# Kernel tuning notes

Hardware: AMD Instinct MI355X
Metric: run time of the kernel (lower is better)

Reference implementation:

```python
import jax, jax.numpy as jnp
import numpy as np

B = 8
INPUT_SIZE = 32        # fc output dim == res row length
RESAMPLING = 500       # chunk width; 500->250->125->62->31 under 4 stride-2 pools
CHUNKS = 15            # == channel_size; seq length T = CHUNKS * RESAMPLING
T = CHUNKS * RESAMPLING
EPS = 1e-5
FC_IN = 32 * 6 * 31    # 5952 = flattened (C,H,W) embedding output


def _conv2d(x, w, b, pad):
    y = jax.lax.conv_general_dilated(x, w, (1, 1), pad,
                                     dimension_numbers=('NCHW', 'OIHW', 'NCHW'))
    return y + b[None, :, None, None]


def _bn(x, g, beta, m, v):
    # eval-mode BatchNorm2d with running stats
    scale = g / jnp.sqrt(v + EPS)
    return (x - m[None, :, None, None]) * scale[None, :, None, None] + beta[None, :, None, None]


def _maxpool22(x):
    return jax.lax.reduce_window(x, -jnp.inf, jax.lax.max, (1, 1, 2, 2), (1, 1, 2, 2), 'VALID')


def _forward(x, w1, b1, g1, beta1, m1, v1, w2, b2, g2, beta2, m2, v2,
             w3, b3, g3, beta3, m3, v3, w4, b4, g4, beta4, m4, v4,
             wfc, bfc, wc3, bc3, wout, bout):
    bsz = x.shape[0]
    # Vectorize the original per-sample / per-chunk Python loops:
    # split each [100, T] sample into CHUNKS windows of width RESAMPLING.
    h = x[:, 0].reshape(bsz, 100, CHUNKS, RESAMPLING)
    h = h.transpose(0, 2, 1, 3).reshape(bsz * CHUNKS, 1, 100, RESAMPLING)
    for w, b, g, bt, m, v in ((w1, b1, g1, beta1, m1, v1),
                              (w2, b2, g2, beta2, m2, v2),
                              (w3, b3, g3, beta3, m3, v3),
                              (w4, b4, g4, beta4, m4, v4)):
        h = _maxpool22(jax.nn.relu(_bn(_conv2d(h, w, b, [(2, 2), (2, 2)]), g, bt, m, v)))
    feats = h.reshape(bsz * CHUNKS, FC_IN)          # torch flattens in (C,H,W) order
    res = feats @ wfc.T + bfc                       # [B*15, 32]
    r = res.reshape(bsz, CHUNKS, INPUT_SIZE)[..., None]  # [B, 15, 32, 1] (NCHW)

    pad_c = lambda t: jnp.pad(t, ((0, 0), (0, 0), (1, 1), (0, 0)))   # ZeroPad2d((0,0,1,1))
    conv3 = lambda t: _conv2d(t, wc3, bc3, [(0, 0), (0, 0)])          # (3,1) conv
    r = conv3(jax.nn.relu(pad_c(r)))
    r = conv3(jax.nn.relu(pad_c(r)))
    while r.shape[2] > 2:  # static shapes: H 32->16->8->4->2
        p = jnp.pad(r, ((0, 0), (0, 0), (0, 1), (0, 0)))              # ZeroPad2d((0,0,0,1))
        px = jax.lax.reduce_window(p, -jnp.inf, jax.lax.max, (1, 1, 3, 1), (1, 1, 2, 2), 'VALID')
        t = conv3(jax.nn.relu(pad_c(px)))
        t = conv3(jax.nn.relu(pad_c(t)))
        r = t + px
    return r.reshape(bsz, 2 * CHUNKS) @ wout.T + bout  # [B, 2]


def setup_inputs() -> dict:
    key = jax.random.key(0)
    ks = jax.random.split(key, 16)

    def rn(k, shape, s):
        return jax.random.normal(k, shape, jnp.float32) * s

    inp = {"x": jax.random.normal(ks[0], (B, 1, 100, T), jnp.float32)}
    chans = [(1, 16), (16, 32), (32, 64), (64, 32)]
    for i, (ci, co) in enumerate(chans, 1):
        inp[f"w{i}"] = rn(ks[i], (co, ci, 5, 5), (2.0 / (ci * 25)) ** 0.5)
        inp[f"b{i}"] = jnp.zeros((co,), jnp.float32)
        inp[f"g{i}"] = jnp.ones((co,), jnp.float32)
        inp[f"beta{i}"] = jnp.zeros((co,), jnp.float32)
        inp[f"m{i}"] = jnp.zeros((co,), jnp.float32)
        inp[f"v{i}"] = jnp.ones((co,), jnp.float32)
    inp["wfc"] = rn(ks[5], (INPUT_SIZE, FC_IN), FC_IN ** -0.5)
    inp["bfc"] = jnp.zeros((INPUT_SIZE,), jnp.float32)
    inp["wc3"] = rn(ks[6], (CHUNKS, CHUNKS, 3, 1), (CHUNKS * 3) ** -0.5)
    inp["bc3"] = jnp.zeros((CHUNKS,), jnp.float32)
    inp["wout"] = rn(ks[7], (2, 2 * CHUNKS), (2 * CHUNKS) ** -0.5)
    inp["bout"] = jnp.zeros((2,), jnp.float32)
    return inp


def reference(x, w1, b1, g1, beta1, m1, v1, w2, b2, g2, beta2, m2, v2,
              w3, b3, g3, beta3, m3, v3, w4, b4, g4, beta4, m4, v4,
              wfc, bfc, wc3, bc3, wout, bout):
    return _forward(x, w1, b1, g1, beta1, m1, v1, w2, b2, g2, beta2, m2, v2,
                    w3, b3, g3, beta3, m3, v3, w4, b4, g4, beta4, m4, v4,
                    wfc, bfc, wc3, bc3, wout, bout)
```

## Files before the change

### kernel.cpp

```cpp
#include <hip/hip_runtime.h>
#include <hip/hip_bf16.h>

#define EPS 1e-5f

typedef short bf16x8 __attribute__((ext_vector_type(8)));
typedef float f32x4  __attribute__((ext_vector_type(4)));

__device__ __forceinline__ unsigned short f2bf(float f) {
    __hip_bfloat16 h = __float2bfloat16(f);
    return *(unsigned short*)&h;
}
__device__ __forceinline__ float bf2f(unsigned short u) {
    __hip_bfloat16 h = *(__hip_bfloat16*)&u;
    return __bfloat162float(h);
}

__global__ void prep_scsh(
    const float* g1, const float* be1, const float* m1, const float* v1, const float* b1,
    const float* g2, const float* be2, const float* m2, const float* v2, const float* b2,
    const float* g3, const float* be3, const float* m3, const float* v3, const float* b3,
    const float* g4, const float* be4, const float* m4, const float* v4, const float* b4,
    float* base)
{
    const int t = threadIdx.x;
    if (t < 32) {
        const float sc = g2[t] / sqrtf(v2[t] + EPS);
        base[t] = sc; base[32 + t] = (b2[t] - m2[t]) * sc + be2[t];
    } else if (t < 96) {
        const int c = t - 32;
        const float sc = g3[c] / sqrtf(v3[c] + EPS);
        base[64 + c] = sc; base[128 + c] = (b3[c] - m3[c]) * sc + be3[c];
    } else if (t < 128) {
        const int c = t - 96;
        const float sc = g4[c] / sqrtf(v4[c] + EPS);
        base[192 + c] = sc; base[224 + c] = (b4[c] - m4[c]) * sc + be4[c];
    } else if (t < 144) {
        const int c = t - 128;
        const float sc = g1[c] / sqrtf(v1[c] + EPS);
        base[256 + c] = sc; base[272 + c] = (b1[c] - m1[c]) * sc + be1[c];
    }
}

template <int CI, int CO, int NP>
__global__ void prep_A(const float* __restrict__ w, unsigned short* __restrict__ Apk)
{
    constexpr int COTALL = CO / 16;
    const int tot = NP * COTALL * 512;
    for (int i = blockIdx.x * 256 + threadIdx.x; i < tot; i += gridDim.x * 256) {
        const int j = i & 7, lane = (i >> 3) & 63, pc = i >> 9;
        const int p = pc / COTALL, cot = pc % COTALL;
        const int kidx = p * 32 + (lane >> 4) * 8 + j;
        const int tap = kidx / CI, ci = kidx % CI;
        const int co = cot * 16 + (lane & 15);
        const float val = (tap < 25) ? w[((size_t)co * CI + ci) * 25 + tap] : 0.f;
        Apk[i] = f2bf(val);
    }
}

__global__ void prep_A1(const float* __restrict__ w, unsigned short* __restrict__ Apk)
{
    const int i = threadIdx.x;
    if (i < 512) {
        const int j = i & 7, lane = i >> 3;
        const int k = ((lane >> 4) & 3) * 8 + j;
        const int co = lane & 15;
        Apk[i] = f2bf((k < 25) ? w[co * 25 + k] : 0.f);
    }
}

__global__ void prep_fcw(const float* __restrict__ wfc, unsigned short* __restrict__ wfcT)
{
    for (int i = blockIdx.x * 256 + threadIdx.x; i < 32 * 5952; i += gridDim.x * 256) {
        const int o = i / 5952, j = i % 5952;
        const int c = j & 31, yx = j >> 5;
        wfcT[i] = f2bf(wfc[(size_t)o * 5952 + c * 186 + yx]);
    }
}

__global__ __launch_bounds__(256) void conv1_mfma(
    const float* __restrict__ x,
    const unsigned short* __restrict__ Apk1,
    const float* __restrict__ sc, const float* __restrict__ sh,
    unsigned short* __restrict__ out)
{
    constexpr int RSTR = 38;
    __shared__ unsigned short tile[12 * RSTR];
    const int n = blockIdx.z;
    const int y0 = blockIdx.y * 8, x0 = blockIdx.x * 32;
    const int b = n / 15, c = n % 15;
    const float* xb = x + (size_t)b * 100 * 7500 + (size_t)c * 500;
    const int tid = threadIdx.x;

    for (int i = tid; i < 12 * 36; i += 256) {
        const int yy = i / 36, xx = i % 36;
        const int gy = y0 - 2 + yy, gx = x0 - 2 + xx;
        float v = 0.f;
        if (gy >= 0 && gy < 100 && gx >= 0 && gx < 500) v = xb[gy * 7500 + gx];
        tile[yy * RSTR + xx] = f2bf(v);
    }

    const int lane = tid & 63, wav = tid >> 6;
    const int g = lane >> 4, c15 = lane & 15;
    const bf16x8 a = *(const bf16x8*)(Apk1 + lane * 8);

    int off[8]; unsigned short msk[8];
    #pragma unroll
    for (int j = 0; j < 8; ++j) {
        int tap = g * 8 + j;
        msk[j] = (tap < 25) ? 0xFFFFu : 0u;
        if (tap > 24) tap = 24;
        off[j] = (tap / 5) * RSTR + (tap % 5);
    }
    __syncthreads();

    f32x4 acc[2][2] = {};
    #pragma unroll
    for (int r = 0; r < 2; ++r)
        #pragma unroll
        for (int cg = 0; cg < 2; ++cg) {
            const int base = (2 * wav + r) * RSTR + cg * 16 + c15;
            bf16x8 bfrag;
            #pragma unroll
            for (int j = 0; j < 8; ++j) {
                const unsigned short v = tile[base + off[j]] & msk[j];
                ((unsigned short*)&bfrag)[j] = (short)v;
            }
            acc[r][cg] = __builtin_amdgcn_mfma_f32_16x16x32_bf16(a, bfrag, acc[r][cg], 0, 0, 0);
        }

    const int py = blockIdx.y * 4 + wav;
    const float4 scv = *(const float4*)(sc + g * 4);
    const float4 shv = *(const float4*)(sh + g * 4);
    #pragma unroll
    for (int cg = 0; cg < 2; ++cg) {
        const int px = (x0 >> 1) + cg * 8 + (c15 >> 1);
        ushort4 st;
        #pragma unroll
        for (int reg = 0; reg < 4; ++reg) {
            const float scr = (&scv.x)[reg], shr = (&shv.x)[reg];
            const float v0 = fmaxf(acc[0][cg][reg] * scr + shr, 0.f);
            const float v1 = fmaxf(acc[1][cg][reg] * scr + shr, 0.f);
            float mx = fmaxf(v0, v1);
            mx = fmaxf(mx, __shfl_xor(mx, 1));
            (&st.x)[reg] = f2bf(mx);
        }
        if ((lane & 1) == 0 && py < 50 && px < 250)
            *(ushort4*)(out + (((size_t)n * 50 + py) * 250 + px) * 16 + g * 4) = st;
    }
}

template <int CI, int CO, int H, int W, int PH, int PW, int NP>
__global__ __launch_bounds__(256) void mfma_conv(
    const unsigned short* __restrict__ in,
    const unsigned short* __restrict__ Apk,
    const float* __restrict__ sc, const float* __restrict__ sh,
    unsigned short* __restrict__ outp)
{
    constexpr int TH = 8, TW = 32, ROWS = TH + 4, COLS = TW + 4;
    constexpr int CSTR = CI * 2 + 16;
    constexpr int COTALL = CO / 16, COB = CO / 32;
    constexpr int CPC = CI / 8;
    __shared__ char smem[ROWS * COLS * CSTR];

    const int n = blockIdx.z / COB, cob = blockIdx.z % COB;
    const int ytile = blockIdx.y * TH, xtile = blockIdx.x * TW;
    const int tid = threadIdx.x;

    for (int i = tid; i < ROWS * COLS * CPC; i += 256) {
        const int cell = i / CPC, ch = i % CPC;
        const int yy = cell / COLS, xx = cell % COLS;
        const int gy = ytile - 2 + yy, gx = xtile - 2 + xx;
        uint4 val = make_uint4(0, 0, 0, 0);
        if (gy >= 0 && gy < H && gx >= 0 && gx < W)
            val = *(const uint4*)(in + ((((size_t)n * H + gy) * W + gx) * CI + ch * 8));
        *(uint4*)(smem + (size_t)(yy * COLS + xx) * CSTR + ch * 16) = val;
    }
    __syncthreads();

    const int lane = tid & 63, wav = tid >> 6;
    const int g = lane >> 4, c15 = lane & 15;
    const int laneCi = (CI == 16) ? ((g & 1) * 16) : (g * 16);
    const bool hi = (lane >= 32);

    int baddr[2][2];
    #pragma unroll
    for (int r = 0; r < 2; ++r)
        #pragma unroll
        for (int cg = 0; cg < 2; ++cg)
            baddr[r][cg] = ((wav * 2 + r) * COLS + cg * 16 + c15) * CSTR + laneCi;

    f32x4 acc[2][2][2] = {};

    #pragma unroll
    for (int p = 0; p < NP; ++p) {
        int D;
        if (CI == 16) {
            int t0 = p * 2;     if (t0 > 24) t0 = 24;
            int t1 = p * 2 + 1; if (t1 > 24) t1 = 24;
            const int D0 = ((t0 / 5) * COLS + t0 % 5) * CSTR;
            const int D1 = ((t1 / 5) * COLS + t1 % 5) * CSTR;
            D = hi ? D1 : D0;
        } else {
            const int tap = (CI == 32) ? p : (p >> 1);
            D = ((tap / 5) * COLS + tap % 5) * CSTR + ((CI == 64) ? (p & 1) * 64 : 0);
        }
        bf16x8 a[2], b[2][2];
        #pragma unroll
        for (int ct = 0; ct < 2; ++ct)
            a[ct] = *(const bf16x8*)(Apk + ((size_t)(p * COTALL + cob * 2 + ct) * 64 + lane) * 8);
        #pragma unroll
        for (int r = 0; r < 2; ++r)
            #pragma unroll
            for (int cg = 0; cg < 2; ++cg)
                b[r][cg] = *(const bf16x8*)(smem + baddr[r][cg] + D);
        #pragma unroll
        for (int r = 0; r < 2; ++r)
            #pragma unroll
            for (int ct = 0; ct < 2; ++ct)
                #pragma unroll
                for (int cg = 0; cg < 2; ++cg)
                    acc[r][ct][cg] = __builtin_amdgcn_mfma_f32_16x16x32_bf16(
                        a[ct], b[r][cg], acc[r][ct][cg], 0, 0, 0);
    }

    const int py = blockIdx.y * 4 + wav;
    #pragma unroll
    for (int ct = 0; ct < 2; ++ct) {
        const int coW = cob * 32 + ct * 16;
        const float4 scv = *(const float4*)(sc + coW + g * 4);
        const float4 shv = *(const float4*)(sh + coW + g * 4);
        #pragma unroll
        for (int cg = 0; cg < 2; ++cg) {
            const int px = (xtile >> 1) + cg * 8 + (c15 >> 1);
            ushort4 st;
            #pragma unroll
            for (int reg = 0; reg < 4; ++reg) {
                const float scr = (&scv.x)[reg], shr = (&shv.x)[reg];
                const float v0 = fmaxf(acc[0][ct][cg][reg] * scr + shr, 0.f);
                const float v1 = fmaxf(acc[1][ct][cg][reg] * scr + shr, 0.f);
                float mx = fmaxf(v0, v1);
                mx = fmaxf(mx, __shfl_xor(mx, 1));
                (&st.x)[reg] = f2bf(mx);
            }
            if ((lane & 1) == 0 && py < PH && px < PW)
                *(ushort4*)(outp + (((size_t)n * PH + py) * PW + px) * CO + coW + g * 4) = st;
        }
    }
}

__global__ __launch_bounds__(256) void fc_kernel(
    const unsigned short* __restrict__ feats, const unsigned short* __restrict__ wfcT,
    const float* __restrict__ bfc, float* __restrict__ res)
{
    const int n = blockIdx.x;
    const int lane = threadIdx.x & 63;
    const int wave = threadIdx.x >> 6;
    const unsigned short* f = feats + (size_t)n * 5952;
    #pragma unroll
    for (int o8 = 0; o8 < 8; ++o8) {
        const int o = wave * 8 + o8;
        const unsigned short* wr = wfcT + (size_t)o * 5952;
        float s = 0.f;
        #pragma unroll
        for (int i = 0; i < 12; ++i) {
            const int j8 = (i * 64 + lane) * 8;
            if (j8 < 5952) {
                const bf16x8 fv = *(const bf16x8*)(f + j8);
                const bf16x8 wv = *(const bf16x8*)(wr + j8);
                #pragma unroll
                for (int q = 0; q < 8; ++q)
                    s += bf2f(((const unsigned short*)&fv)[q]) *
                         bf2f(((const unsigned short*)&wv)[q]);
            }
        }
        #pragma unroll
        for (int off = 32; off > 0; off >>= 1) s += __shfl_down(s, off, 64);
        if (lane == 0) res[n * 32 + o] = s + bfc[o];
    }
}

__global__ __launch_bounds__(512) void dpcnn_kernel(
    const float* __restrict__ res,
    const float* __restrict__ wc3, const float* __restrict__ bc3,
    const float* __restrict__ wout, const float* __restrict__ bout,
    float* __restrict__ out)
{
    __shared__ float rr[8][15][32];
    __shared__ float ar[8][15][34];
    __shared__ float tr[8][15][34];
    __shared__ float px[8][15][16];
    __shared__ float wk[15][45];
    __shared__ float bk[15];

    const int tid = threadIdx.x;
    for (int i = tid; i < 15 * 45; i += 512) ((float*)wk)[i] = wc3[i];
    if (tid < 15) bk[tid] = bc3[tid];
    for (int i = tid; i < 8 * 15 * 32; i += 512) {
        const int h = i & 31, c = (i >> 5) % 15, b = i / 480;
        const float val = res[i];
        rr[b][c][h] = val;
        ar[b][c][h + 1] = fmaxf(val, 0.f);
    }
    for (int i = tid; i < 8 * 15; i += 512) {
        const int c = i % 15, b = i / 15;
        ar[b][c][0] = 0.f; ar[b][c][33] = 0.f;
        tr[b][c][0] = 0.f; tr[b][c][33] = 0.f;
    }
    __syncthreads();

    #define CONV45(SRC, BCH, CCH, HH)                                          \
        float s0 = bk[CCH], s1 = 0.f, s2 = 0.f;                                \
        {                                                                      \
            const float* srow = &SRC[BCH][0][HH];                              \
            const float* wrow = &wk[CCH][0];                                   \
            _Pragma("unroll")                                                  \
            for (int ci = 0; ci < 15; ++ci) {                                  \
                s0 += wrow[ci * 3 + 0] * srow[ci * 34 + 0];                    \
                s1 += wrow[ci * 3 + 1] * srow[ci * 34 + 1];                    \
                s2 += wrow[ci * 3 + 2] * srow[ci * 34 + 2];                    \
            }                                                                  \
        }                                                                      \
        const float val = s0 + s1 + s2;

    {
        for (int i = tid; i < 8 * 15 * 32; i += 512) {
            const int h = i & 31, cc = (i >> 5) % 15, b = i / 480;
            CONV45(ar, b, cc, h)
            tr[b][cc][h + 1] = fmaxf(val, 0.f);
        }
        __syncthreads();
        for (int i = tid; i < 8 * 15 * 32; i += 512) {
            const int h = i & 31, cc = (i >> 5) % 15, b = i / 480;
            CONV45(tr, b, cc, h)
            rr[b][cc][h] = val;
            ar[b][cc][h + 1] = fmaxf(val, 0.f);
        }
        __syncthreads();
    }

    for (int H = 32; H > 2; H >>= 1) {
        const int Hh = H >> 1;
        const int NE = 8 * 15 * Hh;
        for (int i = tid; i < NE; i += 512) {
            const int h = i % Hh, cc = (i / Hh) % 15, b = i / (15 * Hh);
            const float m0 = rr[b][cc][2 * h], m1 = rr[b][cc][2 * h + 1];
            const float m2 = (2 * h + 2 < H) ? rr[b][cc][2 * h + 2] : 0.f;
            const float pv = fmaxf(fmaxf(m0, m1), m2);
            px[b][cc][h] = pv;
            ar[b][cc][h + 1] = fmaxf(pv, 0.f);
            if (h == 0) ar[b][cc][0] = 0.f;
            if (h == Hh - 1) ar[b][cc][Hh + 1] = 0.f;
        }
        __syncthreads();
        for (int i = tid; i < NE; i += 512) {
            const int h = i % Hh, cc = (i / Hh) % 15, b = i / (15 * Hh);
            CONV45(ar, b, cc, h)
            tr[b][cc][h + 1] = fmaxf(val, 0.f);
            if (h == 0) tr[b][cc][0] = 0.f;
            if (h == Hh - 1) tr[b][cc][Hh + 1] = 0.f;
        }
        __syncthreads();
        for (int i = tid; i < NE; i += 512) {
            const int h = i % Hh, cc = (i / Hh) % 15, b = i / (15 * Hh);
            CONV45(tr, b, cc, h)
            const float rv = val + px[b][cc][h];
            rr[b][cc][h] = rv;
            ar[b][cc][h + 1] = fmaxf(rv, 0.f);
        }
        __syncthreads();
    }
    #undef CONV45

    if (tid < 16) {
        const int b = tid >> 1, o = tid & 1;
        float s = bout[o];
        for (int c = 0; c < 15; ++c)
            #pragma unroll
            for (int h = 0; h < 2; ++h)
                s += wout[o * 30 + c * 2 + h] * rr[b][c][h];
        out[b * 2 + o] = s;
    }
}

extern "C" void kernel_launch(void* const* d_in, const int* in_sizes, int n_in,
                              void* d_out, int out_size, void* d_ws, size_t ws_size,
                              hipStream_t stream)
{
    const float* x = (const float*)d_in[0];
    const float* w1 = (const float*)d_in[1];  const float* b1 = (const float*)d_in[2];
    const float* g1 = (const float*)d_in[3];  const float* be1 = (const float*)d_in[4];
    const float* m1 = (const float*)d_in[5];  const float* v1 = (const float*)d_in[6];
    const float* w2 = (const float*)d_in[7];  const float* b2 = (const float*)d_in[8];
    const float* g2 = (const float*)d_in[9];  const float* be2 = (const float*)d_in[10];
    const float* m2 = (const float*)d_in[11]; const float* v2 = (const float*)d_in[12];
    const float* w3 = (const float*)d_in[13]; const float* b3 = (const float*)d_in[14];
    const float* g3 = (const float*)d_in[15]; const float* be3 = (const float*)d_in[16];
    const float* m3 = (const float*)d_in[17]; const float* v3 = (const float*)d_in[18];
    const float* w4 = (const float*)d_in[19]; const float* b4 = (const float*)d_in[20];
    const float* g4 = (const float*)d_in[21]; const float* be4 = (const float*)d_in[22];
    const float* m4 = (const float*)d_in[23]; const float* v4 = (const float*)d_in[24];
    const float* wfc = (const float*)d_in[25]; const float* bfc = (const float*)d_in[26];
    const float* wc3 = (const float*)d_in[27]; const float* bc3 = (const float*)d_in[28];
    const float* wout = (const float*)d_in[29]; const float* bout = (const float*)d_in[30];
    float* out = (float*)d_out;

    (void)in_sizes; (void)n_in; (void)out_size; (void)ws_size;

    float* wsf = (float*)d_ws;
    float* res   = wsf;
    float* scsh  = wsf + 3840;
    float* sc2 = scsh, *sh2 = scsh + 32;
    float* sc3 = scsh + 64, *sh3 = scsh + 128;
    float* sc4 = scsh + 192, *sh4 = scsh + 224;
    float* sc1 = scsh + 256, *sh1 = scsh + 272;
    unsigned short* A1  = (unsigned short*)(wsf + 4160);
    unsigned short* A2  = (unsigned short*)(wsf + 4416);
    unsigned short* A3  = (unsigned short*)(wsf + 11072);
    unsigned short* A4  = (unsigned short*)(wsf + 36672);
    unsigned short* c1o = (unsigned short*)(wsf + 62272);
    unsigned short* c2o = (unsigned short*)(wsf + 12062272);
    unsigned short* c3o = (unsigned short*)(wsf + 18062272);
    unsigned short* c4o = (unsigned short*)(wsf + 20919232);
    unsigned short* wfcT = (unsigned short*)(wsf + 21276352);

    prep_scsh<<<1, 256, 0, stream>>>(g1, be1, m1, v1, b1,
                                     g2, be2, m2, v2, b2,
                                     g3, be3, m3, v3, b3,
                                     g4, be4, m4, v4, b4, scsh);
    prep_A1<<<1, 512, 0, stream>>>(w1, A1);
    prep_A<16, 32, 13><<<52, 256, 0, stream>>>(w2, A2);
    prep_A<32, 64, 25><<<200, 256, 0, stream>>>(w3, A3);
    prep_A<64, 32, 50><<<200, 256, 0, stream>>>(w4, A4);
    prep_fcw<<<744, 256, 0, stream>>>(wfc, wfcT);

    conv1_mfma<<<dim3(16, 13, 120), 256, 0, stream>>>(x, A1, sc1, sh1, c1o);
    mfma_conv<16, 32, 50, 250, 25, 125, 13><<<dim3(8, 7, 120), 256, 0, stream>>>(
        c1o, A2, sc2, sh2, c2o);
    mfma_conv<32, 64, 25, 125, 12, 62, 25><<<dim3(4, 3, 240), 256, 0, stream>>>(
        c2o, A3, sc3, sh3, c3o);
    mfma_conv<64, 32, 12, 62, 6, 31, 50><<<dim3(2, 2, 120), 256, 0, stream>>>(
        c3o, A4, sc4, sh4, c4o);
    fc_kernel<<<dim3(120), 256, 0, stream>>>(c4o, wfcT, bfc, res);
    dpcnn_kernel<<<dim3(1), 512, 0, stream>>>(res, wc3, bc3, wout, bout, out);
}
```

Before: 352.1 us.

## Fuse prep kernels, widen conv1 tile, plane-major LDS layout, full-CO blocks for conv3

Merges the six weight/BN preparation kernels into a single launch to cut launch overhead. conv1 now processes 64-column tiles with four column groups per wave and drops the redundant tap mask, since zero weights cover the padded taps. The generic conv stores its input tile in per-8-channel planes with padding and uses compile-time offsets, which is meant to reduce LDS bank conflicts and address math. Conv3 blocks now compute all 64 output channels, so each input tile is loaded once rather than twice, at the cost of more accumulator registers and half as many blocks.

New measurement: 322.8 us. -8.3%, faster.

```diff
diff --git a/kernel.cpp b/kernel.cpp
--- a/kernel.cpp
+++ b/kernel.cpp
@@ -15,62 +15,62 @@
     return __bfloat162float(h);
 }
 
-__global__ void prep_scsh(
+__device__ __forceinline__ void packA(const float* __restrict__ w,
+                                      unsigned short* __restrict__ Apk,
+                                      int i, int CI, int COTALL)
+{
+    const int j = i & 7, lane = (i >> 3) & 63, pc = i >> 9;
+    const int p = pc / COTALL, cot = pc % COTALL;
+    const int kidx = p * 32 + (lane >> 4) * 8 + j;
+    const int tap = kidx / CI, ci = kidx % CI;
+    const int co = cot * 16 + (lane & 15);
+    Apk[i] = f2bf((tap < 25) ? w[((size_t)co * CI + ci) * 25 + tap] : 0.f);
+}
+
+__global__ void prep_all(
+    const float* w1, const float* w2, const float* w3, const float* w4,
+    const float* wfc,
     const float* g1, const float* be1, const float* m1, const float* v1, const float* b1,
     const float* g2, const float* be2, const float* m2, const float* v2, const float* b2,
     const float* g3, const float* be3, const float* m3, const float* v3, const float* b3,
     const float* g4, const float* be4, const float* m4, const float* v4, const float* b4,
-    float* base)
-{
-    const int t = threadIdx.x;
-    if (t < 32) {
-        const float sc = g2[t] / sqrtf(v2[t] + EPS);
-        base[t] = sc; base[32 + t] = (b2[t] - m2[t]) * sc + be2[t];
-    } else if (t < 96) {
-        const int c = t - 32;
-        const float sc = g3[c] / sqrtf(v3[c] + EPS);
-        base[64 + c] = sc; base[128 + c] = (b3[c] - m3[c]) * sc + be3[c];
-    } else if (t < 128) {
-        const int c = t - 96;
-        const float sc = g4[c] / sqrtf(v4[c] + EPS);
-        base[192 + c] = sc; base[224 + c] = (b4[c] - m4[c]) * sc + be4[c];
-    } else if (t < 144) {
-        const int c = t - 128;
-        const float sc = g1[c] / sqrtf(v1[c] + EPS);
-        base[256 + c] = sc; base[272 + c] = (b1[c] - m1[c]) * sc + be1[c];
-    }
-}
-
-template <int CI, int CO, int NP>
-__global__ void prep_A(const float* __restrict__ w, unsigned short* __restrict__ Apk)
-{
-    constexpr int COTALL = CO / 16;
-    const int tot = NP * COTALL * 512;
-    for (int i = blockIdx.x * 256 + threadIdx.x; i < tot; i += gridDim.x * 256) {
-        const int j = i & 7, lane = (i >> 3) & 63, pc = i >> 9;
-        const int p = pc / COTALL, cot = pc % COTALL;
-        const int kidx = p * 32 + (lane >> 4) * 8 + j;
-        const int tap = kidx / CI, ci = kidx % CI;
-        const int co = cot * 16 + (lane & 15);
-        const float val = (tap < 25) ? w[((size_t)co * CI + ci) * 25 + tap] : 0.f;
-        Apk[i] = f2bf(val);
-    }
-}
-
-__global__ void prep_A1(const float* __restrict__ w, unsigned short* __restrict__ Apk)
-{
-    const int i = threadIdx.x;
-    if (i < 512) {
+    float* scsh, unsigned short* A1, unsigned short* A2, unsigned short* A3,
+    unsigned short* A4, unsigned short* wfcT)
+{
+    constexpr int S0 = 144, S1 = S0 + 512, S2 = S1 + 13312;
+    constexpr int S3 = S2 + 51200, S4 = S3 + 51200, S5 = S4 + 190464;
+    const int idx = blockIdx.x * 256 + threadIdx.x;
+    if (idx < S0) {
+        const int t = idx;
+        if (t < 32) {
+            const float sc = g2[t] / sqrtf(v2[t] + EPS);
+            scsh[t] = sc; scsh[32 + t] = (b2[t] - m2[t]) * sc + be2[t];
+        } else if (t < 96) {
+            const int c = t - 32;
+            const float sc = g3[c] / sqrtf(v3[c] + EPS);
+            scsh[64 + c] = sc; scsh[128 + c] = (b3[c] - m3[c]) * sc + be3[c];
+        } else if (t < 128) {
+            const int c = t - 96;
+            const float sc = g4[c] / sqrtf(v4[c] + EPS);
+            scsh[192 + c] = sc; scsh[224 + c] = (b4[c] - m4[c]) * sc + be4[c];
+        } else {
+            const int c = t - 128;
+            const float sc = g1[c] / sqrtf(v1[c] + EPS);
+            scsh[256 + c] = sc; scsh[272 + c] = (b1[c] - m1[c]) * sc + be1[c];
+        }
+    } else if (idx < S1) {
+        const int i = idx - S0;
         const int j = i & 7, lane = i >> 3;
         const int k = ((lane >> 4) & 3) * 8 + j;
-        const int co = lane & 15;
-        Apk[i] = f2bf((k < 25) ? w[co * 25 + k] : 0.f);
-    }
-}
-
-__global__ void prep_fcw(const float* __restrict__ wfc, unsigned short* __restrict__ wfcT)
-{
-    for (int i = blockIdx.x * 256 + threadIdx.x; i < 32 * 5952; i += gridDim.x * 256) {
+        A1[i] = f2bf((k < 25) ? w1[(lane & 15) * 25 + k] : 0.f);
+    } else if (idx < S2) {
+        packA(w2, A2, idx - S1, 16, 2);
+    } else if (idx < S3) {
+        packA(w3, A3, idx - S2, 32, 4);
+    } else if (idx < S4) {
+        packA(w4, A4, idx - S3, 64, 2);
+    } else if (idx < S5) {
+        const int i = idx - S4;
         const int o = i / 5952, j = i % 5952;
         const int c = j & 31, yx = j >> 5;
         wfcT[i] = f2bf(wfc[(size_t)o * 5952 + c * 186 + yx]);
@@ -83,16 +83,16 @@
     const float* __restrict__ sc, const float* __restrict__ sh,
     unsigned short* __restrict__ out)
 {
-    constexpr int RSTR = 38;
+    constexpr int RSTR = 70;
     __shared__ unsigned short tile[12 * RSTR];
     const int n = blockIdx.z;
-    const int y0 = blockIdx.y * 8, x0 = blockIdx.x * 32;
+    const int y0 = blockIdx.y * 8, x0 = blockIdx.x * 64;
     const int b = n / 15, c = n % 15;
     const float* xb = x + (size_t)b * 100 * 7500 + (size_t)c * 500;
     const int tid = threadIdx.x;
 
-    for (int i = tid; i < 12 * 36; i += 256) {
-        const int yy = i / 36, xx = i % 36;
+    for (int i = tid; i < 12 * 68; i += 256) {
+        const int yy = i / 68, xx = i % 68;
         const int gy = y0 - 2 + yy, gx = x0 - 2 + xx;
         float v = 0.f;
         if (gy >= 0 && gy < 100 && gx >= 0 && gx < 500) v = xb[gy * 7500 + gx];
@@ -103,28 +103,25 @@
     const int g = lane >> 4, c15 = lane & 15;
     const bf16x8 a = *(const bf16x8*)(Apk1 + lane * 8);
 
-    int off[8]; unsigned short msk[8];
+    int off[8];
     #pragma unroll
     for (int j = 0; j < 8; ++j) {
         int tap = g * 8 + j;
-        msk[j] = (tap < 25) ? 0xFFFFu : 0u;
         if (tap > 24) tap = 24;
         off[j] = (tap / 5) * RSTR + (tap % 5);
     }
     __syncthreads();
 
-    f32x4 acc[2][2] = {};
+    f32x4 acc[2][4] = {};
     #pragma unroll
     for (int r = 0; r < 2; ++r)
         #pragma unroll
-        for (int cg = 0; cg < 2; ++cg) {
+        for (int cg = 0; cg < 4; ++cg) {
             const int base = (2 * wav + r) * RSTR + cg * 16 + c15;
             bf16x8 bfrag;
             #pragma unroll
-            for (int j = 0; j < 8; ++j) {
-                const unsigned short v = tile[base + off[j]] & msk[j];
-                ((unsigned short*)&bfrag)[j] = (short)v;
-            }
+            for (int j = 0; j < 8; ++j)
+                ((unsigned short*)&bfrag)[j] = (short)tile[base + off[j]];
             acc[r][cg] = __builtin_amdgcn_mfma_f32_16x16x32_bf16(a, bfrag, acc[r][cg], 0, 0, 0);
         }
 
@@ -132,7 +129,7 @@
     const float4 scv = *(const float4*)(sc + g * 4);
     const float4 shv = *(const float4*)(sh + g * 4);
     #pragma unroll
-    for (int cg = 0; cg < 2; ++cg) {
+    for (int cg = 0; cg < 4; ++cg) {
         const int px = (x0 >> 1) + cg * 8 + (c15 >> 1);
         ushort4 st;
         #pragma unroll
@@ -149,7 +146,7 @@
     }
 }
 
-template <int CI, int CO, int H, int W, int PH, int PW, int NP>
+template <int CI, int CO, int H, int W, int PH, int PW, int NP, int NCT>
 __global__ __launch_bounds__(256) void mfma_conv(
     const unsigned short* __restrict__ in,
     const unsigned short* __restrict__ Apk,
@@ -157,10 +154,13 @@
     unsigned short* __restrict__ outp)
 {
     constexpr int TH = 8, TW = 32, ROWS = TH + 4, COLS = TW + 4;
-    constexpr int CSTR = CI * 2 + 16;
-    constexpr int COTALL = CO / 16, COB = CO / 32;
     constexpr int CPC = CI / 8;
-    __shared__ char smem[ROWS * COLS * CSTR];
+    constexpr int PLANESZ = ROWS * COLS * 16;
+    constexpr int PPAD = (CPC == 2) ? 64 : (CPC == 4 ? 32 : 16);
+    constexpr int PSTR = PLANESZ + PPAD;
+    constexpr int COTALL = CO / 16;
+    constexpr int COB = CO / (16 * NCT);
+    __shared__ char smem[CPC * PSTR];
 
     const int n = blockIdx.z / COB, cob = blockIdx.z % COB;
     const int ytile = blockIdx.y * TH, xtile = blockIdx.x * TW;
@@ -173,50 +173,49 @@
         uint4 val = make_uint4(0, 0, 0, 0);
         if (gy >= 0 && gy < H && gx >= 0 && gx < W)
             val = *(const uint4*)(in + ((((size_t)n * H + gy) * W + gx) * CI + ch * 8));
-        *(uint4*)(smem + (size_t)(yy * COLS + xx) * CSTR + ch * 16) = val;
+        *(uint4*)(smem + ch * PSTR + cell * 16) = val;
     }
     __syncthreads();
 
     const int lane = tid & 63, wav = tid >> 6;
     const int g = lane >> 4, c15 = lane & 15;
-    const int laneCi = (CI == 16) ? ((g & 1) * 16) : (g * 16);
     const bool hi = (lane >= 32);
-
-    int baddr[2][2];
-    #pragma unroll
-    for (int r = 0; r < 2; ++r)
-        #pragma unroll
-        for (int cg = 0; cg < 2; ++cg)
-            baddr[r][cg] = ((wav * 2 + r) * COLS + cg * 16 + c15) * CSTR + laneCi;
-
-    f32x4 acc[2][2][2] = {};
+    const int plane = (CI == 16) ? (g & 1) : g;
+    const char* bbase = smem + plane * PSTR + ((wav * 2) * COLS + c15) * 16;
+
+    f32x4 acc[2][NCT][2] = {};
 
     #pragma unroll
     for (int p = 0; p < NP; ++p) {
-        int D;
+        int Dv = 0;
         if (CI == 16) {
             int t0 = p * 2;     if (t0 > 24) t0 = 24;
             int t1 = p * 2 + 1; if (t1 > 24) t1 = 24;
-            const int D0 = ((t0 / 5) * COLS + t0 % 5) * CSTR;
-            const int D1 = ((t1 / 5) * COLS + t1 % 5) * CSTR;
-            D = hi ? D1 : D0;
-        } else {
-            const int tap = (CI == 32) ? p : (p >> 1);
-            D = ((tap / 5) * COLS + tap % 5) * CSTR + ((CI == 64) ? (p & 1) * 64 : 0);
-        }
-        bf16x8 a[2], b[2][2];
-        #pragma unroll
-        for (int ct = 0; ct < 2; ++ct)
-            a[ct] = *(const bf16x8*)(Apk + ((size_t)(p * COTALL + cob * 2 + ct) * 64 + lane) * 8);
+            const int D0 = ((t0 / 5) * COLS + t0 % 5) * 16;
+            const int D1 = ((t1 / 5) * COLS + t1 % 5) * 16;
+            Dv = hi ? D1 : D0;
+        }
+        const int tap = (CI == 32) ? p : ((CI == 64) ? (p >> 1) : 0);
+        const int pimm = (CI == 64) ? (p & 1) * 4 * PSTR : 0;
+
+        bf16x8 a[NCT], b[2][2];
+        #pragma unroll
+        for (int ct = 0; ct < NCT; ++ct)
+            a[ct] = *(const bf16x8*)(Apk +
+                ((size_t)(p * COTALL + cob * NCT + ct) * 64 + lane) * 8);
         #pragma unroll
         for (int r = 0; r < 2; ++r)
             #pragma unroll
-            for (int cg = 0; cg < 2; ++cg)
-                b[r][cg] = *(const bf16x8*)(smem + baddr[r][cg] + D);
+            for (int cg = 0; cg < 2; ++cg) {
+                const int imm = (CI == 16)
+                    ? (r * COLS + cg * 16) * 16
+                    : (((r + tap / 5) * COLS + cg * 16 + tap % 5) * 16 + pimm);
+                b[r][cg] = *(const bf16x8*)(bbase + Dv + imm);
+            }
         #pragma unroll
         for (int r = 0; r < 2; ++r)
             #pragma unroll
-            for (int ct = 0; ct < 2; ++ct)
+            for (int ct = 0; ct < NCT; ++ct)
                 #pragma unroll
                 for (int cg = 0; cg < 2; ++cg)
                     acc[r][ct][cg] = __builtin_amdgcn_mfma_f32_16x16x32_bf16(
@@ -225,8 +224,8 @@
 
     const int py = blockIdx.y * 4 + wav;
     #pragma unroll
-    for (int ct = 0; ct < 2; ++ct) {
-        const int coW = cob * 32 + ct * 16;
+    for (int ct = 0; ct < NCT; ++ct) {
+        const int coW = (cob * NCT + ct) * 16;
         const float4 scv = *(const float4*)(sc + coW + g * 4);
         const float4 shv = *(const float4*)(sh + coW + g * 4);
         #pragma unroll
@@ -423,22 +422,18 @@
     unsigned short* c4o = (unsigned short*)(wsf + 20919232);
     unsigned short* wfcT = (unsigned short*)(wsf + 21276352);
 
-    prep_scsh<<<1, 256, 0, stream>>>(g1, be1, m1, v1, b1,
-                                     g2, be2, m2, v2, b2,
-                                     g3, be3, m3, v3, b3,
-                                     g4, be4, m4, v4, b4, scsh);
-    prep_A1<<<1, 512, 0, stream>>>(w1, A1);
-    prep_A<16, 32, 13><<<52, 256, 0, stream>>>(w2, A2);
-    prep_A<32, 64, 25><<<200, 256, 0, stream>>>(w3, A3);
-    prep_A<64, 32, 50><<<200, 256, 0, stream>>>(w4, A4);
-    prep_fcw<<<744, 256, 0, stream>>>(wfc, wfcT);
-
-    conv1_mfma<<<dim3(16, 13, 120), 256, 0, stream>>>(x, A1, sc1, sh1, c1o);
-    mfma_conv<16, 32, 50, 250, 25, 125, 13><<<dim3(8, 7, 120), 256, 0, stream>>>(
+    prep_all<<<1199, 256, 0, stream>>>(
+        w1, w2, w3, w4, wfc,
+        g1, be1, m1, v1, b1, g2, be2, m2, v2, b2,
+        g3, be3, m3, v3, b3, g4, be4, m4, v4, b4,
+        scsh, A1, A2, A3, A4, wfcT);
+
+    conv1_mfma<<<dim3(8, 13, 120), 256, 0, stream>>>(x, A1, sc1, sh1, c1o);
+    mfma_conv<16, 32, 50, 250, 25, 125, 13, 2><<<dim3(8, 7, 120), 256, 0, stream>>>(
         c1o, A2, sc2, sh2, c2o);
-    mfma_conv<32, 64, 25, 125, 12, 62, 25><<<dim3(4, 3, 240), 256, 0, stream>>>(
+    mfma_conv<32, 64, 25, 125, 12, 62, 25, 4><<<dim3(4, 3, 120), 256, 0, stream>>>(
         c2o, A3, sc3, sh3, c3o);
-    mfma_conv<64, 32, 12, 62, 6, 31, 50><<<dim3(2, 2, 120), 256, 0, stream>>>(
+    mfma_conv<64, 32, 12, 62, 6, 31, 50, 2><<<dim3(2, 2, 120), 256, 0, stream>>>(
         c3o, A4, sc4, sh4, c4o);
     fc_kernel<<<dim3(120), 256, 0, stream>>>(c4o, wfcT, bfc, res);
     dpcnn_kernel<<<dim3(1), 512, 0, stream>>>(res, wc3, bc3, wout, bout, out);
```
